# Kernel tuning notes

Hardware: AMD Instinct MI355X
Metric: run time of the kernel (lower is better)

The kernel has to match this reference:

```python
import jax, jax.numpy as jnp
import numpy as np

V, D, T, L, H = 65, 64, 32, 4, 4
HD = D // H  # head size 16
FF = 4 * D
EPS = 1e-5


def setup_inputs() -> dict:
    key = jax.random.key(0)
    ks = jax.random.split(key, 24)
    B = 8192
    s = 0.02
    inp = {
        "idx": jax.random.randint(ks[0], (B, T), 0, V, dtype=jnp.int64 if jax.config.jax_enable_x64 else jnp.int32),
        "targets": jax.random.randint(ks[1], (B, T), 0, V, dtype=jnp.int64 if jax.config.jax_enable_x64 else jnp.int32),
        "tok_emb": jax.random.normal(ks[2], (V, D), jnp.float32) * s,
        "pos_emb": jax.random.normal(ks[3], (T, D), jnp.float32) * s,
        # per-layer stacked params (heads' separate Q/K/V Linears concatenated -> [D, D])
        "Wq": jax.random.normal(ks[4], (L, D, D), jnp.float32) * s,
        "Wk": jax.random.normal(ks[5], (L, D, D), jnp.float32) * s,
        "Wv": jax.random.normal(ks[6], (L, D, D), jnp.float32) * s,
        "Wo": jax.random.normal(ks[7], (L, D, D), jnp.float32) * s,
        "bo": jnp.zeros((L, D), jnp.float32),
        "ln1_g": jnp.ones((L, D), jnp.float32),
        "ln1_b": jnp.zeros((L, D), jnp.float32),
        "ln2_g": jnp.ones((L, D), jnp.float32),
        "ln2_b": jnp.zeros((L, D), jnp.float32),
        "W1": jax.random.normal(ks[8], (L, D, FF), jnp.float32) * s,
        "b1": jnp.zeros((L, FF), jnp.float32),
        "W2": jax.random.normal(ks[9], (L, FF, D), jnp.float32) * s,
        "b2": jnp.zeros((L, D), jnp.float32),
        "lnf_g": jnp.ones((D,), jnp.float32),
        "lnf_b": jnp.zeros((D,), jnp.float32),
        "Wh": jax.random.normal(ks[10], (D, V), jnp.float32) * s,
        "bh": jnp.zeros((V,), jnp.float32),
    }
    return inp


def _ln(x, g, b):
    mu = jnp.mean(x, axis=-1, keepdims=True)
    var = jnp.mean(jnp.square(x - mu), axis=-1, keepdims=True)
    return (x - mu) * jax.lax.rsqrt(var + EPS) * g + b


def _attn(x, Wq, Wk, Wv, Wo, bo):
    B, Tt, _ = x.shape
    q = (x @ Wq).reshape(B, Tt, H, HD).transpose(0, 2, 1, 3)  # [B,H,T,hd]
    k = (x @ Wk).reshape(B, Tt, H, HD).transpose(0, 2, 1, 3)
    v = (x @ Wv).reshape(B, Tt, H, HD).transpose(0, 2, 1, 3)
    # NOTE: original scales by C**-0.5 with C = n_embd (64), not head_size
    scores = jnp.einsum("bhqd,bhkd->bhqk", q, k) * (D ** -0.5)
    mask = jnp.tril(jnp.ones((Tt, Tt), bool))
    scores = jnp.where(mask, scores, -jnp.inf)
    wei = jax.nn.softmax(scores, axis=-1)
    out = jnp.einsum("bhqk,bhkd->bhqd", wei, v)
    out = out.transpose(0, 2, 1, 3).reshape(B, Tt, D)  # concat heads
    return out @ Wo + bo


def reference(idx, targets, tok_emb, pos_emb, Wq, Wk, Wv, Wo, bo,
              ln1_g, ln1_b, ln2_g, ln2_b, W1, b1, W2, b2, lnf_g, lnf_b, Wh, bh):
    B, Tt = idx.shape
    x = tok_emb[idx] + pos_emb[:Tt]  # [B,T,D]
    for l in range(L):
        x = x + _attn(_ln(x, ln1_g[l], ln1_b[l]), Wq[l], Wk[l], Wv[l], Wo[l], bo[l])
        h = jax.nn.relu(_ln(x, ln2_g[l], ln2_b[l]) @ W1[l] + b1[l])
        x = x + h @ W2[l] + b2[l]
    x = _ln(x, lnf_g, lnf_b)
    logits = x @ Wh + bh  # [B,T,V]
    logp = jax.nn.log_softmax(logits.reshape(B * Tt, V), axis=-1)
    loss = -jnp.mean(jnp.take_along_axis(logp, targets.reshape(B * Tt, 1), axis=1))
    return logits, loss
```

## Files before the change

### kernel.cpp

```cpp
#include <hip/hip_runtime.h>

typedef unsigned short u16;
typedef __attribute__((ext_vector_type(8))) short bf16x8;
typedef __attribute__((ext_vector_type(4))) float f32x4;

#define NV 65
#define ND 64
#define NT 32
#define NL 4
#define NH 4
#define NFF 256
#define NSEQ 8192
#define NTOK (NSEQ * NT)

#define WQT_OFF 0
#define WKT_OFF 16384
#define WVT_OFF 32768
#define WOT_OFF 49152
#define W1T_OFF 65536
#define W2T_OFF 131072
#define WHT_OFF 196608
#define WS_U16_TOTAL 201728
#define LOSS_BYTE_OFF (WS_U16_TOTAL * 2)

__device__ __forceinline__ u16 f2bf(float f) {
  union { float f; unsigned u; } c; c.f = f;
  return (u16)((c.u + 0x7FFFu + ((c.u >> 16) & 1u)) >> 16);
}
__device__ __forceinline__ float bf2f(u16 h) {
  union { unsigned u; float f; } c; c.u = ((unsigned)h) << 16;
  return c.f;
}
__device__ __forceinline__ f32x4 zero4() {
  f32x4 z; z[0] = 0.f; z[1] = 0.f; z[2] = 0.f; z[3] = 0.f; return z;
}

__global__ void prep_kernel(const float* __restrict__ Wq, const float* __restrict__ Wk,
                            const float* __restrict__ Wv, const float* __restrict__ Wo,
                            const float* __restrict__ W1, const float* __restrict__ W2,
                            const float* __restrict__ Wh, u16* __restrict__ ws,
                            float* __restrict__ loss_acc) {
  int i = blockIdx.x * 256 + threadIdx.x;
  if (i == 0) *loss_acc = 0.f;
  if (i < 16384) {
    int lay = i >> 12, j = i & 4095, n = j >> 6, k = j & 63;
    int src = (lay << 12) + (k << 6) + n;
    ws[WQT_OFF + i] = f2bf(Wq[src]);
    ws[WKT_OFF + i] = f2bf(Wk[src]);
    ws[WVT_OFF + i] = f2bf(Wv[src]);
    ws[WOT_OFF + i] = f2bf(Wo[src]);
  }
  if (i < 65536) {
    int lay = i >> 14, j = i & 16383;
    { int n = j >> 6, k = j & 63;   ws[W1T_OFF + i] = f2bf(W1[(lay << 14) + (k << 8) + n]); }
    { int n = j >> 8, k = j & 255;  ws[W2T_OFF + i] = f2bf(W2[(lay << 14) + (k << 6) + n]); }
  }
  if (i < 5120) {
    int n = i >> 6, k = i & 63;
    ws[WHT_OFF + i] = (n < NV) ? f2bf(Wh[k * NV + n]) : (u16)0;
  }
}

__device__ __forceinline__ void layer_norm(const u16 (*src)[72], u16 (*dst)[72],
                                           const float* __restrict__ g, const float* __restrict__ b,
                                           float* mu_s, float* rs_s, int l) {
  int r = l >> 1, c0 = (l & 1) * 32;
  float s = 0.f, sq = 0.f;
#pragma unroll
  for (int c8 = 0; c8 < 4; ++c8) {
    bf16x8 v8 = *(const bf16x8*)&src[r][c0 + c8 * 8];
#pragma unroll
    for (int j = 0; j < 8; ++j) {
      float v = bf2f((u16)v8[j]);
      s += v; sq += v * v;
    }
  }
  s += __shfl_xor(s, 1); sq += __shfl_xor(sq, 1);
  if (!(l & 1)) {
    float mu = s * (1.f / 64.f);
    float var = sq * (1.f / 64.f) - mu * mu;
    mu_s[r] = mu;
    rs_s[r] = rsqrtf(var + 1e-5f);
  }
  __syncthreads();
  float ga = g[l], be = b[l];
#pragma unroll 4
  for (int rr = 0; rr < NT; ++rr) {
    float v = bf2f(src[rr][l]);
    dst[rr][l] = f2bf((v - mu_s[rr]) * rs_s[rr] * ga + be);
  }
  __syncthreads();
}

__global__ __launch_bounds__(64) void fwd_kernel(
    const int* __restrict__ idx, const int* __restrict__ tgt,
    const float* __restrict__ tok_emb, const float* __restrict__ pos_emb,
    const float* __restrict__ bo, const float* __restrict__ ln1g, const float* __restrict__ ln1b,
    const float* __restrict__ ln2g, const float* __restrict__ ln2b,
    const float* __restrict__ b1, const float* __restrict__ b2,
    const float* __restrict__ lnfg, const float* __restrict__ lnfb, const float* __restrict__ bh,
    const u16* __restrict__ ws, float* __restrict__ out, float* __restrict__ loss_acc) {
  __shared__ u16 xs[NT][72];
  __shared__ u16 ls[NT][72];
  __shared__ u16 tp[NT][72];
  __shared__ u16 qp[NT][40];
  __shared__ u16 kh[NT][40];
  __shared__ u16 vt[16][40];
  __shared__ float mu_s[NT];
  __shared__ float rs_s[NT];

  const int l = threadIdx.x;
  const int m = l & 15, g = l >> 4;
  const int seq = blockIdx.x;
  const int row_g = 4 * g;

  {
    int r = l >> 1, c0 = 16 + (l & 1) * 8;
#pragma unroll
    for (int c = 0; c < 8; ++c) kh[r][c0 + c] = 0;
  }
  const int* idxp = idx + seq * NT;
#pragma unroll 4
  for (int r = 0; r < NT; ++r) {
    int t = idxp[r];
    xs[r][l] = f2bf(tok_emb[t * ND + l] + pos_emb[r * ND + l]);
  }
  __syncthreads();

  for (int lay = 0; lay < NL; ++lay) {
    const u16* wq = ws + WQT_OFF + lay * 4096;
    const u16* wk = ws + WKT_OFF + lay * 4096;
    const u16* wv = ws + WVT_OFF + lay * 4096;
    const u16* wo = ws + WOT_OFF + lay * 4096;
    const u16* w1 = ws + W1T_OFF + lay * 16384;
    const u16* w2 = ws + W2T_OFF + lay * 16384;

    layer_norm(xs, ls, ln1g + lay * ND, ln1b + lay * ND, mu_s, rs_s, l);

    bf16x8 a_ls[2][2];
#pragma unroll
    for (int mt = 0; mt < 2; ++mt)
#pragma unroll
      for (int ks = 0; ks < 2; ++ks)
        a_ls[mt][ks] = *(const bf16x8*)&ls[16 * mt + m][32 * ks + 8 * g];

    for (int h = 0; h < NH; ++h) {
      f32x4 qa[2], ka[2], va[2];
#pragma unroll
      for (int mt = 0; mt < 2; ++mt) { qa[mt] = zero4(); ka[mt] = zero4(); va[mt] = zero4(); }
#pragma unroll
      for (int ks = 0; ks < 2; ++ks) {
        int wrow = (16 * h + m) * 64 + 32 * ks + 8 * g;
        bf16x8 bq = *(const bf16x8*)&wq[wrow];
        bf16x8 bk = *(const bf16x8*)&wk[wrow];
        bf16x8 bv = *(const bf16x8*)&wv[wrow];
#pragma unroll
        for (int mt = 0; mt < 2; ++mt) {
          qa[mt] = __builtin_amdgcn_mfma_f32_16x16x32_bf16(a_ls[mt][ks], bq, qa[mt], 0, 0, 0);
          ka[mt] = __builtin_amdgcn_mfma_f32_16x16x32_bf16(a_ls[mt][ks], bk, ka[mt], 0, 0, 0);
          va[mt] = __builtin_amdgcn_mfma_f32_16x16x32_bf16(a_ls[mt][ks], bv, va[mt], 0, 0, 0);
        }
      }
      __syncthreads();
#pragma unroll
      for (int mt = 0; mt < 2; ++mt)
#pragma unroll
        for (int r = 0; r < 4; ++r) {
          int tok = 16 * mt + row_g + r;
          qp[tok][m] = f2bf(qa[mt][r]);
          qp[tok][16 + m] = 0;
          kh[tok][m] = f2bf(ka[mt][r]);
          vt[m][tok] = f2bf(va[mt][r]);
        }
      __syncthreads();
      f32x4 sc[2][2];
#pragma unroll
      for (int mt = 0; mt < 2; ++mt) { sc[mt][0] = zero4(); sc[mt][1] = zero4(); }
      bf16x8 bk0 = *(const bf16x8*)&kh[m][8 * g];
      bf16x8 bk1 = *(const bf16x8*)&kh[16 + m][8 * g];
#pragma unroll
      for (int mt = 0; mt < 2; ++mt) {
        bf16x8 aq = *(const bf16x8*)&qp[16 * mt + m][8 * g];
        sc[mt][0] = __builtin_amdgcn_mfma_f32_16x16x32_bf16(aq, bk0, sc[mt][0], 0, 0, 0);
        sc[mt][1] = __builtin_amdgcn_mfma_f32_16x16x32_bf16(aq, bk1, sc[mt][1], 0, 0, 0);
      }
#pragma unroll
      for (int mt = 0; mt < 2; ++mt)
#pragma unroll
        for (int r = 0; r < 4; ++r) {
          int tok = 16 * mt + row_g + r;
          float s0 = sc[mt][0][r] * 0.125f; if (m > tok) s0 = -1e30f;
          float s1 = sc[mt][1][r] * 0.125f; if (16 + m > tok) s1 = -1e30f;
          float mx = fmaxf(s0, s1);
          mx = fmaxf(mx, __shfl_xor(mx, 1));
          mx = fmaxf(mx, __shfl_xor(mx, 2));
          mx = fmaxf(mx, __shfl_xor(mx, 4));
          mx = fmaxf(mx, __shfl_xor(mx, 8));
          float e0 = __expf(s0 - mx), e1 = __expf(s1 - mx);
          float sm = e0 + e1;
          sm += __shfl_xor(sm, 1); sm += __shfl_xor(sm, 2);
          sm += __shfl_xor(sm, 4); sm += __shfl_xor(sm, 8);
          float inv = 1.f / sm;
          qp[tok][m] = f2bf(e0 * inv);
          qp[tok][16 + m] = f2bf(e1 * inv);
        }
      __syncthreads();
      bf16x8 bv2 = *(const bf16x8*)&vt[m][8 * g];
#pragma unroll
      for (int mt = 0; mt < 2; ++mt) {
        bf16x8 ap = *(const bf16x8*)&qp[16 * mt + m][8 * g];
        f32x4 o = zero4();
        o = __builtin_amdgcn_mfma_f32_16x16x32_bf16(ap, bv2, o, 0, 0, 0);
#pragma unroll
        for (int r = 0; r < 4; ++r)
          tp[16 * mt + row_g + r][16 * h + m] = f2bf(o[r]);
      }
    }
    __syncthreads();
    {
      f32x4 acc[2][4];
#pragma unroll
      for (int mt = 0; mt < 2; ++mt)
#pragma unroll
        for (int nt = 0; nt < 4; ++nt) acc[mt][nt] = zero4();
      bf16x8 a_t[2][2];
#pragma unroll
      for (int mt = 0; mt < 2; ++mt)
#pragma unroll
        for (int ks = 0; ks < 2; ++ks)
          a_t[mt][ks] = *(const bf16x8*)&tp[16 * mt + m][32 * ks + 8 * g];
#pragma unroll
      for (int ks = 0; ks < 2; ++ks)
#pragma unroll
        for (int nt = 0; nt < 4; ++nt) {
          bf16x8 bw = *(const bf16x8*)&wo[(16 * nt + m) * 64 + 32 * ks + 8 * g];
#pragma unroll
          for (int mt = 0; mt < 2; ++mt)
            acc[mt][nt] = __builtin_amdgcn_mfma_f32_16x16x32_bf16(a_t[mt][ks], bw, acc[mt][nt], 0, 0, 0);
        }
#pragma unroll
      for (int nt = 0; nt < 4; ++nt) {
        float bon = bo[lay * ND + 16 * nt + m];
#pragma unroll
        for (int mt = 0; mt < 2; ++mt)
#pragma unroll
          for (int r = 0; r < 4; ++r) {
            int tok = 16 * mt + row_g + r, col = 16 * nt + m;
            xs[tok][col] = f2bf(acc[mt][nt][r] + bon + bf2f(xs[tok][col]));
          }
      }
    }
    __syncthreads();
    layer_norm(xs, ls, ln2g + lay * ND, ln2b + lay * ND, mu_s, rs_s, l);
    {
      bf16x8 a_l2[2][2];
#pragma unroll
      for (int mt = 0; mt < 2; ++mt)
#pragma unroll
        for (int ks = 0; ks < 2; ++ks)
          a_l2[mt][ks] = *(const bf16x8*)&ls[16 * mt + m][32 * ks + 8 * g];
      f32x4 acc2[2][4];
#pragma unroll
      for (int mt = 0; mt < 2; ++mt)
#pragma unroll
        for (int nt = 0; nt < 4; ++nt) acc2[mt][nt] = zero4();
      for (int c = 0; c < 4; ++c) {
        f32x4 hc[2][4];
#pragma unroll
        for (int mt = 0; mt < 2; ++mt)
#pragma unroll
          for (int nt = 0; nt < 4; ++nt) hc[mt][nt] = zero4();
#pragma unroll
        for (int ks = 0; ks < 2; ++ks)
#pragma unroll
          for (int nt = 0; nt < 4; ++nt) {
            bf16x8 bw = *(const bf16x8*)&w1[(64 * c + 16 * nt + m) * 64 + 32 * ks + 8 * g];
#pragma unroll
            for (int mt = 0; mt < 2; ++mt)
              hc[mt][nt] = __builtin_amdgcn_mfma_f32_16x16x32_bf16(a_l2[mt][ks], bw, hc[mt][nt], 0, 0, 0);
          }
        __syncthreads();
#pragma unroll
        for (int nt = 0; nt < 4; ++nt) {
          float b1n = b1[lay * NFF + 64 * c + 16 * nt + m];
#pragma unroll
          for (int mt = 0; mt < 2; ++mt)
#pragma unroll
            for (int r = 0; r < 4; ++r)
              tp[16 * mt + row_g + r][16 * nt + m] = f2bf(fmaxf(hc[mt][nt][r] + b1n, 0.f));
        }
        __syncthreads();
        bf16x8 a_h[2][2];
#pragma unroll
        for (int mt = 0; mt < 2; ++mt)
#pragma unroll
          for (int ks = 0; ks < 2; ++ks)
            a_h[mt][ks] = *(const bf16x8*)&tp[16 * mt + m][32 * ks + 8 * g];
#pragma unroll
        for (int ks = 0; ks < 2; ++ks)
#pragma unroll
          for (int nt = 0; nt < 4; ++nt) {
            bf16x8 bw = *(const bf16x8*)&w2[(16 * nt + m) * NFF + 64 * c + 32 * ks + 8 * g];
#pragma unroll
            for (int mt = 0; mt < 2; ++mt)
              acc2[mt][nt] = __builtin_amdgcn_mfma_f32_16x16x32_bf16(a_h[mt][ks], bw, acc2[mt][nt], 0, 0, 0);
          }
      }
#pragma unroll
      for (int nt = 0; nt < 4; ++nt) {
        float b2n = b2[lay * ND + 16 * nt + m];
#pragma unroll
        for (int mt = 0; mt < 2; ++mt)
#pragma unroll
          for (int r = 0; r < 4; ++r) {
            int tok = 16 * mt + row_g + r, col = 16 * nt + m;
            xs[tok][col] = f2bf(acc2[mt][nt][r] + b2n + bf2f(xs[tok][col]));
          }
      }
    }
    __syncthreads();
  }

  layer_norm(xs, ls, lnfg, lnfb, mu_s, rs_s, l);
  bf16x8 a_f[2][2];
#pragma unroll
  for (int mt = 0; mt < 2; ++mt)
#pragma unroll
    for (int ks = 0; ks < 2; ++ks)
      a_f[mt][ks] = *(const bf16x8*)&ls[16 * mt + m][32 * ks + 8 * g];
  f32x4 lg[2][5];
#pragma unroll
  for (int mt = 0; mt < 2; ++mt)
#pragma unroll
    for (int nt = 0; nt < 5; ++nt) lg[mt][nt] = zero4();
#pragma unroll
  for (int ks = 0; ks < 2; ++ks)
#pragma unroll
    for (int nt = 0; nt < 5; ++nt) {
      bf16x8 bw = *(const bf16x8*)&ws[WHT_OFF + (16 * nt + m) * 64 + 32 * ks + 8 * g];
#pragma unroll
      for (int mt = 0; mt < 2; ++mt)
        lg[mt][nt] = __builtin_amdgcn_mfma_f32_16x16x32_bf16(a_f[mt][ks], bw, lg[mt][nt], 0, 0, 0);
    }
  const int* tgp = tgt + seq * NT;
  float lloss = 0.f;
#pragma unroll
  for (int mt = 0; mt < 2; ++mt)
#pragma unroll
    for (int r = 0; r < 4; ++r) {
      int tok = 16 * mt + row_g + r;
      float val[5];
      float mx = -1e30f;
#pragma unroll
      for (int nt = 0; nt < 5; ++nt) {
        int cc = 16 * nt + m;
        float v = (cc < NV) ? (lg[mt][nt][r] + bh[cc < NV ? cc : 0]) : -1e30f;
        val[nt] = v;
        mx = fmaxf(mx, v);
      }
      mx = fmaxf(mx, __shfl_xor(mx, 1));
      mx = fmaxf(mx, __shfl_xor(mx, 2));
      mx = fmaxf(mx, __shfl_xor(mx, 4));
      mx = fmaxf(mx, __shfl_xor(mx, 8));
      float se = 0.f;
#pragma unroll
      for (int nt = 0; nt < 5; ++nt) se += __expf(val[nt] - mx);
      se += __shfl_xor(se, 1); se += __shfl_xor(se, 2);
      se += __shfl_xor(se, 4); se += __shfl_xor(se, 8);
      float lse = __logf(se) + mx;
      int t = tgp[tok];
      float tpv = 0.f;
#pragma unroll
      for (int nt = 0; nt < 5; ++nt) tpv += (16 * nt + m == t) ? val[nt] : 0.f;
      float tv = __shfl(tpv, 16 * g + (t & 15));
      if (m == 0) lloss += lse - tv;
      size_t obase = ((size_t)seq * NT + tok) * NV;
#pragma unroll
      for (int nt = 0; nt < 5; ++nt) {
        int cc = 16 * nt + m;
        if (cc < NV) out[obase + cc] = val[nt];
      }
    }
  lloss += __shfl_xor(lloss, 16);
  lloss += __shfl_xor(lloss, 32);
  if (l == 0) atomicAdd(loss_acc, lloss);
}

__global__ void finalize_kernel(const float* __restrict__ loss_acc, float* __restrict__ out) {
  if (threadIdx.x == 0 && blockIdx.x == 0)
    out[(size_t)NTOK * NV] = loss_acc[0] * (1.f / (float)NTOK);
}

extern "C" void kernel_launch(void* const* d_in, const int* in_sizes, int n_in,
                              void* d_out, int out_size, void* d_ws, size_t ws_size,
                              hipStream_t stream) {
  const int* idx = (const int*)d_in[0];
  const int* tgt = (const int*)d_in[1];
  const float* tok_emb = (const float*)d_in[2];
  const float* pos_emb = (const float*)d_in[3];
  const float* Wq = (const float*)d_in[4];
  const float* Wk = (const float*)d_in[5];
  const float* Wv = (const float*)d_in[6];
  const float* Wo = (const float*)d_in[7];
  const float* bo = (const float*)d_in[8];
  const float* ln1g = (const float*)d_in[9];
  const float* ln1b = (const float*)d_in[10];
  const float* ln2g = (const float*)d_in[11];
  const float* ln2b = (const float*)d_in[12];
  const float* W1 = (const float*)d_in[13];
  const float* b1 = (const float*)d_in[14];
  const float* W2 = (const float*)d_in[15];
  const float* b2 = (const float*)d_in[16];
  const float* lnfg = (const float*)d_in[17];
  const float* lnfb = (const float*)d_in[18];
  const float* Wh = (const float*)d_in[19];
  const float* bh = (const float*)d_in[20];
  u16* ws = (u16*)d_ws;
  float* loss_acc = (float*)((char*)d_ws + LOSS_BYTE_OFF);
  float* out = (float*)d_out;

  prep_kernel<<<256, 256, 0, stream>>>(Wq, Wk, Wv, Wo, W1, W2, Wh, ws, loss_acc);
  fwd_kernel<<<NSEQ, 64, 0, stream>>>(idx, tgt, tok_emb, pos_emb, bo, ln1g, ln1b, ln2g, ln2b,
                                      b1, b2, lnfg, lnfb, bh, ws, out, loss_acc);
  finalize_kernel<<<1, 64, 0, stream>>>(loss_acc, out);
}
```

Baseline: 598.1 us.

## Fuse layernorm into MFMA fragments, prefetch weights, and streamline softmax reductions

```diff
diff --git a/kernel.cpp b/kernel.cpp
--- a/kernel.cpp
+++ b/kernel.cpp
@@ -1,8 +1,10 @@
 #include <hip/hip_runtime.h>
 
 typedef unsigned short u16;
+typedef unsigned int u32;
 typedef __attribute__((ext_vector_type(8))) short bf16x8;
 typedef __attribute__((ext_vector_type(4))) float f32x4;
+typedef __attribute__((ext_vector_type(2))) unsigned u32x2;
 
 #define NV 65
 #define ND 64
@@ -23,16 +25,30 @@
 #define WS_U16_TOTAL 201728
 #define LOSS_BYTE_OFF (WS_U16_TOTAL * 2)
 
-__device__ __forceinline__ u16 f2bf(float f) {
-  union { float f; unsigned u; } c; c.f = f;
-  return (u16)((c.u + 0x7FFFu + ((c.u >> 16) & 1u)) >> 16);
-}
-__device__ __forceinline__ float bf2f(u16 h) {
-  union { unsigned u; float f; } c; c.u = ((unsigned)h) << 16;
-  return c.f;
-}
+#define MFMA(a, b, c) __builtin_amdgcn_mfma_f32_16x16x32_bf16(a, b, c, 0, 0, 0)
+
+__device__ __forceinline__ u32 cvtpk(float lo, float hi) {
+  u32 r;
+  asm("v_cvt_pk_bf16_f32 %0, %1, %2" : "=v"(r) : "v"(lo), "v"(hi));
+  return r;
+}
+__device__ __forceinline__ u16 f2bf(float f) { return (u16)cvtpk(f, f); }
+__device__ __forceinline__ float asf(u32 u) { union { u32 u; float f; } c; c.u = u; return c.f; }
+__device__ __forceinline__ float bf2f(u16 h) { return asf(((u32)h) << 16); }
 __device__ __forceinline__ f32x4 zero4() {
   f32x4 z; z[0] = 0.f; z[1] = 0.f; z[2] = 0.f; z[3] = 0.f; return z;
+}
+template <int CTRL>
+__device__ __forceinline__ float dpp_add(float x) {
+  int yi = __builtin_amdgcn_update_dpp(0, __float_as_int(x), CTRL, 0xf, 0xf, true);
+  return x + __int_as_float(yi);
+}
+__device__ __forceinline__ float red16(float x) {
+  x = dpp_add<0xB1>(x);
+  x = dpp_add<0x4E>(x);
+  x = dpp_add<0x141>(x);
+  x = dpp_add<0x140>(x);
+  return x;
 }
 
 __global__ void prep_kernel(const float* __restrict__ Wq, const float* __restrict__ Wk,
@@ -52,8 +68,8 @@
   }
   if (i < 65536) {
     int lay = i >> 14, j = i & 16383;
-    { int n = j >> 6, k = j & 63;   ws[W1T_OFF + i] = f2bf(W1[(lay << 14) + (k << 8) + n]); }
-    { int n = j >> 8, k = j & 255;  ws[W2T_OFF + i] = f2bf(W2[(lay << 14) + (k << 6) + n]); }
+    { int n = j >> 6, k = j & 63;  ws[W1T_OFF + i] = f2bf(W1[(lay << 14) + (k << 8) + n]); }
+    { int n = j >> 8, k = j & 255; ws[W2T_OFF + i] = f2bf(W2[(lay << 14) + (k << 6) + n]); }
   }
   if (i < 5120) {
     int n = i >> 6, k = i & 63;
@@ -61,38 +77,65 @@
   }
 }
 
-__device__ __forceinline__ void layer_norm(const u16 (*src)[72], u16 (*dst)[72],
-                                           const float* __restrict__ g, const float* __restrict__ b,
-                                           float* mu_s, float* rs_s, int l) {
+__device__ __forceinline__ void ln_stats(const u16 (*src)[72], float* murs_s, float* rs_s, int l) {
   int r = l >> 1, c0 = (l & 1) * 32;
   float s = 0.f, sq = 0.f;
 #pragma unroll
   for (int c8 = 0; c8 < 4; ++c8) {
-    bf16x8 v8 = *(const bf16x8*)&src[r][c0 + c8 * 8];
-#pragma unroll
-    for (int j = 0; j < 8; ++j) {
-      float v = bf2f((u16)v8[j]);
-      s += v; sq += v * v;
-    }
-  }
-  s += __shfl_xor(s, 1); sq += __shfl_xor(sq, 1);
+    union { bf16x8 h; u32 u[4]; } w;
+    w.h = *(const bf16x8*)&src[r][c0 + 8 * c8];
+#pragma unroll
+    for (int p = 0; p < 4; ++p) {
+      float lo = asf(w.u[p] << 16), hi = asf(w.u[p] & 0xffff0000u);
+      s += lo + hi;
+      sq = fmaf(lo, lo, sq);
+      sq = fmaf(hi, hi, sq);
+    }
+  }
+  s = dpp_add<0xB1>(s);
+  sq = dpp_add<0xB1>(sq);
   if (!(l & 1)) {
-    float mu = s * (1.f / 64.f);
-    float var = sq * (1.f / 64.f) - mu * mu;
-    mu_s[r] = mu;
-    rs_s[r] = rsqrtf(var + 1e-5f);
+    float mu = s * 0.015625f;
+    float var = fmaf(sq, 0.015625f, -mu * mu);
+    float rs = __builtin_amdgcn_rsqf(var + 1e-5f);
+    rs_s[r] = rs;
+    murs_s[r] = mu * rs;
   }
   __syncthreads();
-  float ga = g[l], be = b[l];
-#pragma unroll 4
-  for (int rr = 0; rr < NT; ++rr) {
-    float v = bf2f(src[rr][l]);
-    dst[rr][l] = f2bf((v - mu_s[rr]) * rs_s[rr] * ga + be);
-  }
-  __syncthreads();
-}
-
-__global__ __launch_bounds__(64) void fwd_kernel(
+}
+
+__device__ __forceinline__ bf16x8 ln_frag(const u16* src, const float* gp, const float* bp,
+                                          float rs, float murs) {
+  union { bf16x8 h; u32 u[4]; } in, out;
+  in.h = *(const bf16x8*)src;
+  f32x4 g0 = *(const f32x4*)gp, g1 = *(const f32x4*)(gp + 4);
+  f32x4 b0 = *(const f32x4*)bp, b1 = *(const f32x4*)(bp + 4);
+  float ga[8] = {g0[0], g0[1], g0[2], g0[3], g1[0], g1[1], g1[2], g1[3]};
+  float ba[8] = {b0[0], b0[1], b0[2], b0[3], b1[0], b1[1], b1[2], b1[3]};
+#pragma unroll
+  for (int p = 0; p < 4; ++p) {
+    float lo = asf(in.u[p] << 16), hi = asf(in.u[p] & 0xffff0000u);
+    lo = fmaf(lo, rs, -murs);
+    hi = fmaf(hi, rs, -murs);
+    out.u[p] = cvtpk(fmaf(lo, ga[2 * p], ba[2 * p]), fmaf(hi, ga[2 * p + 1], ba[2 * p + 1]));
+  }
+  return out.h;
+}
+
+#define BUILD_LN_FRAGS(dst, gbase, bbase)                                      \
+  {                                                                            \
+    float rs0 = rs_s[m], mm0 = murs_s[m];                                      \
+    float rs1 = rs_s[16 + m], mm1 = murs_s[16 + m];                            \
+    _Pragma("unroll")                                                          \
+    for (int ks = 0; ks < 2; ++ks) {                                           \
+      const float* gp = (gbase) + 32 * ks + 8 * g;                             \
+      const float* bp = (bbase) + 32 * ks + 8 * g;                             \
+      dst[0][ks] = ln_frag(&xs[m][32 * ks + 8 * g], gp, bp, rs0, mm0);         \
+      dst[1][ks] = ln_frag(&xs[16 + m][32 * ks + 8 * g], gp, bp, rs1, mm1);    \
+    }                                                                          \
+  }
+
+__global__ __launch_bounds__(64, 3) void fwd_kernel(
     const int* __restrict__ idx, const int* __restrict__ tgt,
     const float* __restrict__ tok_emb, const float* __restrict__ pos_emb,
     const float* __restrict__ bo, const float* __restrict__ ln1g, const float* __restrict__ ln1b,
@@ -101,29 +144,44 @@
     const float* __restrict__ lnfg, const float* __restrict__ lnfb, const float* __restrict__ bh,
     const u16* __restrict__ ws, float* __restrict__ out, float* __restrict__ loss_acc) {
   __shared__ u16 xs[NT][72];
-  __shared__ u16 ls[NT][72];
   __shared__ u16 tp[NT][72];
   __shared__ u16 qp[NT][40];
   __shared__ u16 kh[NT][40];
   __shared__ u16 vt[16][40];
-  __shared__ float mu_s[NT];
+  __shared__ float murs_s[NT];
   __shared__ float rs_s[NT];
 
   const int l = threadIdx.x;
   const int m = l & 15, g = l >> 4;
+  const int row_g = 4 * g;
   const int seq = blockIdx.x;
-  const int row_g = 4 * g;
 
   {
     int r = l >> 1, c0 = 16 + (l & 1) * 8;
-#pragma unroll
-    for (int c = 0; c < 8; ++c) kh[r][c0 + c] = 0;
-  }
-  const int* idxp = idx + seq * NT;
-#pragma unroll 4
-  for (int r = 0; r < NT; ++r) {
-    int t = idxp[r];
-    xs[r][l] = f2bf(tok_emb[t * ND + l] + pos_emb[r * ND + l]);
+    u32x2 zz; zz[0] = 0u; zz[1] = 0u;
+    *(u32x2*)&qp[r][c0] = zz;
+    *(u32x2*)&qp[r][c0 + 4] = zz;
+    *(u32x2*)&kh[r][c0] = zz;
+    *(u32x2*)&kh[r][c0 + 4] = zz;
+  }
+  {
+    int r = l >> 1, c0 = (l & 1) * 32;
+    int t = idx[seq * NT + r];
+    const float* te = tok_emb + t * ND + c0;
+    const float* pe = pos_emb + r * ND + c0;
+#pragma unroll
+    for (int q8 = 0; q8 < 4; ++q8) {
+      f32x4 a0 = *(const f32x4*)(te + 8 * q8);
+      f32x4 a1 = *(const f32x4*)(te + 8 * q8 + 4);
+      f32x4 p0 = *(const f32x4*)(pe + 8 * q8);
+      f32x4 p1 = *(const f32x4*)(pe + 8 * q8 + 4);
+      union { bf16x8 h; u32 u[4]; } o;
+      o.u[0] = cvtpk(a0[0] + p0[0], a0[1] + p0[1]);
+      o.u[1] = cvtpk(a0[2] + p0[2], a0[3] + p0[3]);
+      o.u[2] = cvtpk(a1[0] + p1[0], a1[1] + p1[1]);
+      o.u[3] = cvtpk(a1[2] + p1[2], a1[3] + p1[3]);
+      *(bf16x8*)&xs[r][c0 + 8 * q8] = o.h;
+    }
   }
   __syncthreads();
 
@@ -135,109 +193,119 @@
     const u16* w1 = ws + W1T_OFF + lay * 16384;
     const u16* w2 = ws + W2T_OFF + lay * 16384;
 
-    layer_norm(xs, ls, ln1g + lay * ND, ln1b + lay * ND, mu_s, rs_s, l);
-
+    ln_stats(xs, murs_s, rs_s, l);
     bf16x8 a_ls[2][2];
-#pragma unroll
-    for (int mt = 0; mt < 2; ++mt)
-#pragma unroll
-      for (int ks = 0; ks < 2; ++ks)
-        a_ls[mt][ks] = *(const bf16x8*)&ls[16 * mt + m][32 * ks + 8 * g];
-
+    BUILD_LN_FRAGS(a_ls, ln1g + lay * ND, ln1b + lay * ND)
+
+    bf16x8 qf0, qf1, kf0, kf1, vf0, vf1;
+    {
+      const u16* p = wq + m * 64 + 8 * g;
+      qf0 = *(const bf16x8*)p; qf1 = *(const bf16x8*)(p + 32);
+      p = wk + m * 64 + 8 * g;
+      kf0 = *(const bf16x8*)p; kf1 = *(const bf16x8*)(p + 32);
+      p = wv + m * 64 + 8 * g;
+      vf0 = *(const bf16x8*)p; vf1 = *(const bf16x8*)(p + 32);
+    }
+#pragma unroll
     for (int h = 0; h < NH; ++h) {
-      f32x4 qa[2], ka[2], va[2];
-#pragma unroll
-      for (int mt = 0; mt < 2; ++mt) { qa[mt] = zero4(); ka[mt] = zero4(); va[mt] = zero4(); }
-#pragma unroll
-      for (int ks = 0; ks < 2; ++ks) {
-        int wrow = (16 * h + m) * 64 + 32 * ks + 8 * g;
-        bf16x8 bq = *(const bf16x8*)&wq[wrow];
-        bf16x8 bk = *(const bf16x8*)&wk[wrow];
-        bf16x8 bv = *(const bf16x8*)&wv[wrow];
-#pragma unroll
-        for (int mt = 0; mt < 2; ++mt) {
-          qa[mt] = __builtin_amdgcn_mfma_f32_16x16x32_bf16(a_ls[mt][ks], bq, qa[mt], 0, 0, 0);
-          ka[mt] = __builtin_amdgcn_mfma_f32_16x16x32_bf16(a_ls[mt][ks], bk, ka[mt], 0, 0, 0);
-          va[mt] = __builtin_amdgcn_mfma_f32_16x16x32_bf16(a_ls[mt][ks], bv, va[mt], 0, 0, 0);
-        }
+      f32x4 qa0 = zero4(), qa1 = zero4(), ka0 = zero4(), ka1 = zero4(), va0 = zero4(), va1 = zero4();
+      qa0 = MFMA(a_ls[0][0], qf0, qa0); qa0 = MFMA(a_ls[0][1], qf1, qa0);
+      qa1 = MFMA(a_ls[1][0], qf0, qa1); qa1 = MFMA(a_ls[1][1], qf1, qa1);
+      ka0 = MFMA(a_ls[0][0], kf0, ka0); ka0 = MFMA(a_ls[0][1], kf1, ka0);
+      ka1 = MFMA(a_ls[1][0], kf0, ka1); ka1 = MFMA(a_ls[1][1], kf1, ka1);
+      va0 = MFMA(a_ls[0][0], vf0, va0); va0 = MFMA(a_ls[0][1], vf1, va0);
+      va1 = MFMA(a_ls[1][0], vf0, va1); va1 = MFMA(a_ls[1][1], vf1, va1);
+      if (h < 3) {
+        const u16* p = wq + (16 * (h + 1) + m) * 64 + 8 * g;
+        qf0 = *(const bf16x8*)p; qf1 = *(const bf16x8*)(p + 32);
+        p = wk + (16 * (h + 1) + m) * 64 + 8 * g;
+        kf0 = *(const bf16x8*)p; kf1 = *(const bf16x8*)(p + 32);
+        p = wv + (16 * (h + 1) + m) * 64 + 8 * g;
+        vf0 = *(const bf16x8*)p; vf1 = *(const bf16x8*)(p + 32);
       }
       __syncthreads();
 #pragma unroll
-      for (int mt = 0; mt < 2; ++mt)
-#pragma unroll
-        for (int r = 0; r < 4; ++r) {
-          int tok = 16 * mt + row_g + r;
-          qp[tok][m] = f2bf(qa[mt][r]);
-          qp[tok][16 + m] = 0;
-          kh[tok][m] = f2bf(ka[mt][r]);
-          vt[m][tok] = f2bf(va[mt][r]);
-        }
+      for (int r = 0; r < 4; ++r) {
+        qp[row_g + r][m] = f2bf(qa0[r] * 0.125f);
+        qp[16 + row_g + r][m] = f2bf(qa1[r] * 0.125f);
+        qp[16 + row_g + r][16 + m] = 0;
+        kh[row_g + r][m] = f2bf(ka0[r]);
+        kh[16 + row_g + r][m] = f2bf(ka1[r]);
+      }
+      {
+        u32x2 w0; w0[0] = cvtpk(va0[0], va0[1]); w0[1] = cvtpk(va0[2], va0[3]);
+        *(u32x2*)&vt[m][row_g] = w0;
+        u32x2 w1v; w1v[0] = cvtpk(va1[0], va1[1]); w1v[1] = cvtpk(va1[2], va1[3]);
+        *(u32x2*)&vt[m][16 + row_g] = w1v;
+      }
       __syncthreads();
-      f32x4 sc[2][2];
-#pragma unroll
-      for (int mt = 0; mt < 2; ++mt) { sc[mt][0] = zero4(); sc[mt][1] = zero4(); }
-      bf16x8 bk0 = *(const bf16x8*)&kh[m][8 * g];
-      bf16x8 bk1 = *(const bf16x8*)&kh[16 + m][8 * g];
-#pragma unroll
-      for (int mt = 0; mt < 2; ++mt) {
-        bf16x8 aq = *(const bf16x8*)&qp[16 * mt + m][8 * g];
-        sc[mt][0] = __builtin_amdgcn_mfma_f32_16x16x32_bf16(aq, bk0, sc[mt][0], 0, 0, 0);
-        sc[mt][1] = __builtin_amdgcn_mfma_f32_16x16x32_bf16(aq, bk1, sc[mt][1], 0, 0, 0);
-      }
-#pragma unroll
-      for (int mt = 0; mt < 2; ++mt)
-#pragma unroll
-        for (int r = 0; r < 4; ++r) {
-          int tok = 16 * mt + row_g + r;
-          float s0 = sc[mt][0][r] * 0.125f; if (m > tok) s0 = -1e30f;
-          float s1 = sc[mt][1][r] * 0.125f; if (16 + m > tok) s1 = -1e30f;
-          float mx = fmaxf(s0, s1);
-          mx = fmaxf(mx, __shfl_xor(mx, 1));
-          mx = fmaxf(mx, __shfl_xor(mx, 2));
-          mx = fmaxf(mx, __shfl_xor(mx, 4));
-          mx = fmaxf(mx, __shfl_xor(mx, 8));
-          float e0 = __expf(s0 - mx), e1 = __expf(s1 - mx);
-          float sm = e0 + e1;
-          sm += __shfl_xor(sm, 1); sm += __shfl_xor(sm, 2);
-          sm += __shfl_xor(sm, 4); sm += __shfl_xor(sm, 8);
-          float inv = 1.f / sm;
-          qp[tok][m] = f2bf(e0 * inv);
-          qp[tok][16 + m] = f2bf(e1 * inv);
-        }
-      __syncthreads();
-      bf16x8 bv2 = *(const bf16x8*)&vt[m][8 * g];
-#pragma unroll
-      for (int mt = 0; mt < 2; ++mt) {
-        bf16x8 ap = *(const bf16x8*)&qp[16 * mt + m][8 * g];
-        f32x4 o = zero4();
-        o = __builtin_amdgcn_mfma_f32_16x16x32_bf16(ap, bv2, o, 0, 0, 0);
-#pragma unroll
-        for (int r = 0; r < 4; ++r)
-          tp[16 * mt + row_g + r][16 * h + m] = f2bf(o[r]);
+      bf16x8 kb0 = *(const bf16x8*)&kh[m][8 * g];
+      bf16x8 kb1 = *(const bf16x8*)&kh[16 + m][8 * g];
+      bf16x8 aq0 = *(const bf16x8*)&qp[m][8 * g];
+      bf16x8 aq1 = *(const bf16x8*)&qp[16 + m][8 * g];
+      f32x4 s00 = zero4(), s10 = zero4(), s11 = zero4();
+      s00 = MFMA(aq0, kb0, s00);
+      s10 = MFMA(aq1, kb0, s10);
+      s11 = MFMA(aq1, kb1, s11);
+      float i0[4], i1[4];
+#pragma unroll
+      for (int r = 0; r < 4; ++r) {
+        int tok = row_g + r;
+        float e0 = (m > tok) ? 0.f : __expf(s00[r]);
+        float sm = red16(e0);
+        i0[r] = __builtin_amdgcn_rcpf(sm);
+        qp[tok][m] = f2bf(e0);
+      }
+#pragma unroll
+      for (int r = 0; r < 4; ++r) {
+        int tok = 16 + row_g + r;
+        float e0 = __expf(s10[r]);
+        float e1 = (16 + m > tok) ? 0.f : __expf(s11[r]);
+        float sm = red16(e0 + e1);
+        i1[r] = __builtin_amdgcn_rcpf(sm);
+        qp[tok][m] = f2bf(e0);
+        qp[tok][16 + m] = f2bf(e1);
+      }
+      bf16x8 vb = *(const bf16x8*)&vt[m][8 * g];
+      bf16x8 ap0 = *(const bf16x8*)&qp[m][8 * g];
+      bf16x8 ap1 = *(const bf16x8*)&qp[16 + m][8 * g];
+      f32x4 o0 = zero4(), o1 = zero4();
+      o0 = MFMA(ap0, vb, o0);
+      o1 = MFMA(ap1, vb, o1);
+#pragma unroll
+      for (int r = 0; r < 4; ++r) {
+        tp[row_g + r][16 * h + m] = f2bf(o0[r] * i0[r]);
+        tp[16 + row_g + r][16 * h + m] = f2bf(o1[r] * i1[r]);
       }
     }
     __syncthreads();
+
     {
-      f32x4 acc[2][4];
-#pragma unroll
-      for (int mt = 0; mt < 2; ++mt)
-#pragma unroll
-        for (int nt = 0; nt < 4; ++nt) acc[mt][nt] = zero4();
+      bf16x8 wof[8];
+#pragma unroll
+      for (int nt = 0; nt < 4; ++nt) {
+        const u16* p = wo + (16 * nt + m) * 64 + 8 * g;
+        wof[2 * nt] = *(const bf16x8*)p;
+        wof[2 * nt + 1] = *(const bf16x8*)(p + 32);
+      }
       bf16x8 a_t[2][2];
 #pragma unroll
       for (int mt = 0; mt < 2; ++mt)
 #pragma unroll
         for (int ks = 0; ks < 2; ++ks)
           a_t[mt][ks] = *(const bf16x8*)&tp[16 * mt + m][32 * ks + 8 * g];
+      f32x4 acc[2][4];
+#pragma unroll
+      for (int mt = 0; mt < 2; ++mt)
+#pragma unroll
+        for (int nt = 0; nt < 4; ++nt) acc[mt][nt] = zero4();
 #pragma unroll
       for (int ks = 0; ks < 2; ++ks)
 #pragma unroll
-        for (int nt = 0; nt < 4; ++nt) {
-          bf16x8 bw = *(const bf16x8*)&wo[(16 * nt + m) * 64 + 32 * ks + 8 * g];
+        for (int nt = 0; nt < 4; ++nt)
 #pragma unroll
           for (int mt = 0; mt < 2; ++mt)
-            acc[mt][nt] = __builtin_amdgcn_mfma_f32_16x16x32_bf16(a_t[mt][ks], bw, acc[mt][nt], 0, 0, 0);
-        }
+            acc[mt][nt] = MFMA(a_t[mt][ks], wof[2 * nt + ks], acc[mt][nt]);
 #pragma unroll
       for (int nt = 0; nt < 4; ++nt) {
         float bon = bo[lay * ND + 16 * nt + m];
@@ -251,135 +319,143 @@
       }
     }
     __syncthreads();
-    layer_norm(xs, ls, ln2g + lay * ND, ln2b + lay * ND, mu_s, rs_s, l);
-    {
-      bf16x8 a_l2[2][2];
+
+    ln_stats(xs, murs_s, rs_s, l);
+    bf16x8 a_l2[2][2];
+    BUILD_LN_FRAGS(a_l2, ln2g + lay * ND, ln2b + lay * ND)
+    f32x4 acc2[2][4];
+#pragma unroll
+    for (int mt = 0; mt < 2; ++mt)
+#pragma unroll
+      for (int nt = 0; nt < 4; ++nt) acc2[mt][nt] = zero4();
+    bf16x8 w1f[8];
+#pragma unroll
+    for (int nt = 0; nt < 4; ++nt) {
+      const u16* p = w1 + (16 * nt + m) * 64 + 8 * g;
+      w1f[2 * nt] = *(const bf16x8*)p;
+      w1f[2 * nt + 1] = *(const bf16x8*)(p + 32);
+    }
+#pragma unroll
+    for (int c = 0; c < 4; ++c) {
+      f32x4 hc[2][4];
 #pragma unroll
       for (int mt = 0; mt < 2; ++mt)
 #pragma unroll
+        for (int nt = 0; nt < 4; ++nt) hc[mt][nt] = zero4();
+#pragma unroll
+      for (int ks = 0; ks < 2; ++ks)
+#pragma unroll
+        for (int nt = 0; nt < 4; ++nt)
+#pragma unroll
+          for (int mt = 0; mt < 2; ++mt)
+            hc[mt][nt] = MFMA(a_l2[mt][ks], w1f[2 * nt + ks], hc[mt][nt]);
+      bf16x8 w2f[8];
+#pragma unroll
+      for (int nt = 0; nt < 4; ++nt) {
+        const u16* p = w2 + (16 * nt + m) * NFF + 64 * c + 8 * g;
+        w2f[2 * nt] = *(const bf16x8*)p;
+        w2f[2 * nt + 1] = *(const bf16x8*)(p + 32);
+      }
+      __syncthreads();
+#pragma unroll
+      for (int nt = 0; nt < 4; ++nt) {
+        float b1n = b1[lay * NFF + 64 * c + 16 * nt + m];
+#pragma unroll
+        for (int mt = 0; mt < 2; ++mt)
+#pragma unroll
+          for (int r = 0; r < 4; ++r)
+            tp[16 * mt + row_g + r][16 * nt + m] = f2bf(fmaxf(hc[mt][nt][r] + b1n, 0.f));
+      }
+      __syncthreads();
+      bf16x8 a_h[2][2];
+#pragma unroll
+      for (int mt = 0; mt < 2; ++mt)
+#pragma unroll
         for (int ks = 0; ks < 2; ++ks)
-          a_l2[mt][ks] = *(const bf16x8*)&ls[16 * mt + m][32 * ks + 8 * g];
-      f32x4 acc2[2][4];
+          a_h[mt][ks] = *(const bf16x8*)&tp[16 * mt + m][32 * ks + 8 * g];
+      if (c < 3) {
+#pragma unroll
+        for (int nt = 0; nt < 4; ++nt) {
+          const u16* p = w1 + (64 * (c + 1) + 16 * nt + m) * 64 + 8 * g;
+          w1f[2 * nt] = *(const bf16x8*)p;
+          w1f[2 * nt + 1] = *(const bf16x8*)(p + 32);
+        }
+      }
+#pragma unroll
+      for (int ks = 0; ks < 2; ++ks)
+#pragma unroll
+        for (int nt = 0; nt < 4; ++nt)
+#pragma unroll
+          for (int mt = 0; mt < 2; ++mt)
+            acc2[mt][nt] = MFMA(a_h[mt][ks], w2f[2 * nt + ks], acc2[mt][nt]);
+    }
+#pragma unroll
+    for (int nt = 0; nt < 4; ++nt) {
+      float b2n = b2[lay * ND + 16 * nt + m];
 #pragma unroll
       for (int mt = 0; mt < 2; ++mt)
 #pragma unroll
-        for (int nt = 0; nt < 4; ++nt) acc2[mt][nt] = zero4();
-      for (int c = 0; c < 4; ++c) {
-        f32x4 hc[2][4];
-#pragma unroll
-        for (int mt = 0; mt < 2; ++mt)
-#pragma unroll
-          for (int nt = 0; nt < 4; ++nt) hc[mt][nt] = zero4();
-#pragma unroll
-        for (int ks = 0; ks < 2; ++ks)
-#pragma unroll
-          for (int nt = 0; nt < 4; ++nt) {
-            bf16x8 bw = *(const bf16x8*)&w1[(64 * c + 16 * nt + m) * 64 + 32 * ks + 8 * g];
-#pragma unroll
-            for (int mt = 0; mt < 2; ++mt)
-              hc[mt][nt] = __builtin_amdgcn_mfma_f32_16x16x32_bf16(a_l2[mt][ks], bw, hc[mt][nt], 0, 0, 0);
-          }
-        __syncthreads();
-#pragma unroll
-        for (int nt = 0; nt < 4; ++nt) {
-          float b1n = b1[lay * NFF + 64 * c + 16 * nt + m];
-#pragma unroll
-          for (int mt = 0; mt < 2; ++mt)
-#pragma unroll
-            for (int r = 0; r < 4; ++r)
-              tp[16 * mt + row_g + r][16 * nt + m] = f2bf(fmaxf(hc[mt][nt][r] + b1n, 0.f));
+        for (int r = 0; r < 4; ++r) {
+          int tok = 16 * mt + row_g + r, col = 16 * nt + m;
+          xs[tok][col] = f2bf(acc2[mt][nt][r] + b2n + bf2f(xs[tok][col]));
         }
-        __syncthreads();
-        bf16x8 a_h[2][2];
-#pragma unroll
-        for (int mt = 0; mt < 2; ++mt)
-#pragma unroll
-          for (int ks = 0; ks < 2; ++ks)
-            a_h[mt][ks] = *(const bf16x8*)&tp[16 * mt + m][32 * ks + 8 * g];
-#pragma unroll
-        for (int ks = 0; ks < 2; ++ks)
-#pragma unroll
-          for (int nt = 0; nt < 4; ++nt) {
-            bf16x8 bw = *(const bf16x8*)&w2[(16 * nt + m) * NFF + 64 * c + 32 * ks + 8 * g];
-#pragma unroll
-            for (int mt = 0; mt < 2; ++mt)
-              acc2[mt][nt] = __builtin_amdgcn_mfma_f32_16x16x32_bf16(a_h[mt][ks], bw, acc2[mt][nt], 0, 0, 0);
-          }
-      }
-#pragma unroll
-      for (int nt = 0; nt < 4; ++nt) {
-        float b2n = b2[lay * ND + 16 * nt + m];
-#pragma unroll
-        for (int mt = 0; mt < 2; ++mt)
-#pragma unroll
-          for (int r = 0; r < 4; ++r) {
-            int tok = 16 * mt + row_g + r, col = 16 * nt + m;
-            xs[tok][col] = f2bf(acc2[mt][nt][r] + b2n + bf2f(xs[tok][col]));
-          }
-      }
     }
     __syncthreads();
   }
 
-  layer_norm(xs, ls, lnfg, lnfb, mu_s, rs_s, l);
+  ln_stats(xs, murs_s, rs_s, l);
   bf16x8 a_f[2][2];
+  BUILD_LN_FRAGS(a_f, lnfg, lnfb)
+  bf16x8 whf[10];
+#pragma unroll
+  for (int nt = 0; nt < 5; ++nt) {
+    const u16* p = ws + WHT_OFF + (16 * nt + m) * 64 + 8 * g;
+    whf[2 * nt] = *(const bf16x8*)p;
+    whf[2 * nt + 1] = *(const bf16x8*)(p + 32);
+  }
+  f32x4 lg[2][5];
 #pragma unroll
   for (int mt = 0; mt < 2; ++mt)
 #pragma unroll
-    for (int ks = 0; ks < 2; ++ks)
-      a_f[mt][ks] = *(const bf16x8*)&ls[16 * mt + m][32 * ks + 8 * g];
-  f32x4 lg[2][5];
-#pragma unroll
-  for (int mt = 0; mt < 2; ++mt)
-#pragma unroll
     for (int nt = 0; nt < 5; ++nt) lg[mt][nt] = zero4();
 #pragma unroll
   for (int ks = 0; ks < 2; ++ks)
 #pragma unroll
-    for (int nt = 0; nt < 5; ++nt) {
-      bf16x8 bw = *(const bf16x8*)&ws[WHT_OFF + (16 * nt + m) * 64 + 32 * ks + 8 * g];
+    for (int nt = 0; nt < 5; ++nt)
 #pragma unroll
       for (int mt = 0; mt < 2; ++mt)
-        lg[mt][nt] = __builtin_amdgcn_mfma_f32_16x16x32_bf16(a_f[mt][ks], bw, lg[mt][nt], 0, 0, 0);
-    }
+        lg[mt][nt] = MFMA(a_f[mt][ks], whf[2 * nt + ks], lg[mt][nt]);
   const int* tgp = tgt + seq * NT;
+  float bh0 = bh[m], bh1 = bh[16 + m], bh2v = bh[32 + m], bh3 = bh[48 + m], bh4 = bh[64];
   float lloss = 0.f;
 #pragma unroll
   for (int mt = 0; mt < 2; ++mt)
 #pragma unroll
     for (int r = 0; r < 4; ++r) {
       int tok = 16 * mt + row_g + r;
-      float val[5];
-      float mx = -1e30f;
-#pragma unroll
-      for (int nt = 0; nt < 5; ++nt) {
-        int cc = 16 * nt + m;
-        float v = (cc < NV) ? (lg[mt][nt][r] + bh[cc < NV ? cc : 0]) : -1e30f;
-        val[nt] = v;
-        mx = fmaxf(mx, v);
-      }
-      mx = fmaxf(mx, __shfl_xor(mx, 1));
-      mx = fmaxf(mx, __shfl_xor(mx, 2));
-      mx = fmaxf(mx, __shfl_xor(mx, 4));
-      mx = fmaxf(mx, __shfl_xor(mx, 8));
-      float se = 0.f;
-#pragma unroll
-      for (int nt = 0; nt < 5; ++nt) se += __expf(val[nt] - mx);
-      se += __shfl_xor(se, 1); se += __shfl_xor(se, 2);
-      se += __shfl_xor(se, 4); se += __shfl_xor(se, 8);
-      float lse = __logf(se) + mx;
+      float v0 = lg[mt][0][r] + bh0;
+      float v1 = lg[mt][1][r] + bh1;
+      float v2 = lg[mt][2][r] + bh2v;
+      float v3 = lg[mt][3][r] + bh3;
+      float v4 = lg[mt][4][r] + bh4;
+      float se = __expf(v0) + __expf(v1) + __expf(v2) + __expf(v3) + ((m == 0) ? __expf(v4) : 0.f);
+      se = red16(se);
+      float lse = __logf(se);
       int t = tgp[tok];
       float tpv = 0.f;
-#pragma unroll
-      for (int nt = 0; nt < 5; ++nt) tpv += (16 * nt + m == t) ? val[nt] : 0.f;
+      tpv += (m == t) ? v0 : 0.f;
+      tpv += (16 + m == t) ? v1 : 0.f;
+      tpv += (32 + m == t) ? v2 : 0.f;
+      tpv += (48 + m == t) ? v3 : 0.f;
+      tpv += (m == 0 && t == 64) ? v4 : 0.f;
       float tv = __shfl(tpv, 16 * g + (t & 15));
       if (m == 0) lloss += lse - tv;
-      size_t obase = ((size_t)seq * NT + tok) * NV;
-#pragma unroll
-      for (int nt = 0; nt < 5; ++nt) {
-        int cc = 16 * nt + m;
-        if (cc < NV) out[obase + cc] = val[nt];
-      }
+      float* ob = out + ((size_t)seq * NT + tok) * NV;
+      ob[m] = v0;
+      ob[16 + m] = v1;
+      ob[32 + m] = v2;
+      ob[48 + m] = v3;
+      if (m == 0) ob[64] = v4;
     }
   lloss += __shfl_xor(lloss, 16);
   lloss += __shfl_xor(lloss, 32);
```

Result: faster. 558.5 us (median of 2 runs) (-6.6%).
